# Performance work log

Hardware: AMD Instinct MI355X
Metric: run time of the kernel (lower is better)

The kernel has to match this reference:

```python
import math
import jax, jax.numpy as jnp
import numpy as np

HEADS = 8
DIM_HEAD = 64
NUM_MEM_KV = 16


def alibi_slopes(heads):
    def pow2_slopes(n):
        start = 2 ** (-(2 ** -(math.log2(n) - 3)))
        return [start * (start ** i) for i in range(n)]
    if math.log2(heads).is_integer():
        return np.asarray(pow2_slopes(heads), dtype=np.float32)
    cp2 = 2 ** math.floor(math.log2(heads))
    extra = pow2_slopes(2 * cp2)[0::2][: heads - cp2]
    return np.asarray(pow2_slopes(cp2) + extra, dtype=np.float32)


def setup_inputs() -> dict:
    key = jax.random.key(0)
    ks = jax.random.split(key, 12)
    b, n, dim = 2, 2048, 512
    h, dh, mem = HEADS, DIM_HEAD, NUM_MEM_KV
    s = 0.02  # weight init scale for numerical sanity
    return {
        "x": jax.random.normal(ks[0], (b, n, dim), jnp.float32),
        "Wq": jax.random.normal(ks[1], (dim, h * dh), jnp.float32) * s,
        "Wk": jax.random.normal(ks[2], (dim, h * dh), jnp.float32) * s,
        "Wv": jax.random.normal(ks[3], (dim, h * dh), jnp.float32) * s,
        "mem_k": jax.random.normal(ks[4], (h, mem, dh), jnp.float32),
        "mem_v": jax.random.normal(ks[5], (h, mem, dh), jnp.float32),
        "pre_proj": jax.random.normal(ks[6], (h, h), jnp.float32),
        "post_proj": jax.random.normal(ks[7], (h, h), jnp.float32),
        "head_scale_params": jnp.ones((1, h, 1, 1), jnp.float32),
        "Wout": jax.random.normal(ks[8], (h * dh, dim), jnp.float32) * s,
        "bout": jnp.zeros((dim,), jnp.float32),
    }


def reference(x, Wq, Wk, Wv, mem_k, mem_v, pre_proj, post_proj,
              head_scale_params, Wout, bout):
    b, n, dim = x.shape
    h, dh, mem = HEADS, DIM_HEAD, NUM_MEM_KV
    scale = dh ** -0.5

    def split_heads(t):  # [b,n,h*dh] -> [b,h,n,dh]
        return t.reshape(b, n, h, dh).transpose(0, 2, 1, 3)

    q = split_heads(x @ Wq)
    k = split_heads(x @ Wk)
    v = split_heads(x @ Wv)

    # prepend learned memory key/values: k,v -> [b,h,mem+n,dh]
    k = jnp.concatenate([jnp.broadcast_to(mem_k, (b, h, mem, dh)), k], axis=2)
    v = jnp.concatenate([jnp.broadcast_to(mem_v, (b, h, mem, dh)), v], axis=2)
    j = mem + n

    dots = jnp.einsum('bhid,bhjd->bhij', q, k) * scale
    # talking heads (pre-softmax)
    dots = jnp.einsum('bhij,hk->bkij', dots, pre_proj)
    # alibi relative positional bias: arange(j) * slope per head
    slopes = jnp.asarray(alibi_slopes(h))  # [h]
    dots = dots + jnp.arange(j, dtype=dots.dtype)[None, None, None, :] * slopes[None, :, None, None]
    # causal mask (mem columns always visible); mask where col-mem > row
    neg = -jnp.finfo(dots.dtype).max
    causal = (jnp.arange(j)[None, :] - mem) > jnp.arange(n)[:, None]  # [n,j]
    dots = jnp.where(causal[None, None], neg, dots)

    attn = jax.nn.softmax(dots, axis=-1)
    # talking heads (post-softmax)
    attn = jnp.einsum('bhij,hk->bkij', attn, post_proj)

    out = jnp.einsum('bhij,bhjd->bhid', attn, v)
    out = out * head_scale_params
    out = out.transpose(0, 2, 1, 3).reshape(b, n, h * dh)
    return out @ Wout + bout
```

## Files before the change

kernel.cpp:

```cpp
#include <hip/hip_runtime.h>
#include <math.h>

namespace {
constexpr int B = 2;
constexpr int N = 2048;
constexpr int DIM = 512;
constexpr int H = 8;
constexpr int MEM = 16;
constexpr int J = MEM + N;
constexpr int CHUNK = 256;
constexpr float S2 = 0.125f * 1.4426950408889634f;
constexpr size_t EPB = 17170432;
}

typedef __attribute__((ext_vector_type(8))) short short8;
typedef __attribute__((ext_vector_type(2))) float floatx2;
typedef __attribute__((ext_vector_type(4))) float floatx4;
typedef __attribute__((ext_vector_type(4))) unsigned short ushortx4;
typedef __attribute__((ext_vector_type(8))) unsigned short ushortx8;

__device__ inline unsigned short f2bf(float f) {
    unsigned int u = __float_as_uint(f);
    u += 0x7fffu + ((u >> 16) & 1u);
    return (unsigned short)(u >> 16);
}
__device__ inline unsigned int pk2bf(float a, float b) {
    return ((__float_as_uint(a) + 0x8000u) >> 16) |
           ((__float_as_uint(b) + 0x8000u) & 0xffff0000u);
}

__global__ __launch_bounds__(256)
void x_conv(const float* __restrict__ x, unsigned short* __restrict__ x16)
{
    const size_t base = ((size_t)blockIdx.x * 256 + threadIdx.x) * 8;
    const float4 a = *(const float4*)(x + base);
    const float4 b = *(const float4*)(x + base + 4);
    ushortx8 o = { f2bf(a.x), f2bf(a.y), f2bf(a.z), f2bf(a.w),
                   f2bf(b.x), f2bf(b.y), f2bf(b.z), f2bf(b.w) };
    *(ushortx8*)(x16 + base) = o;
}

__global__ __launch_bounds__(256)
void wt_conv(const float* __restrict__ Wq, const float* __restrict__ Wk,
             const float* __restrict__ Wv, const float* __restrict__ Wo,
             unsigned short* __restrict__ tq, unsigned short* __restrict__ tk,
             unsigned short* __restrict__ tv, unsigned short* __restrict__ to_)
{
    const int z = blockIdx.z;
    const float* __restrict__ W = (z == 0) ? Wq : (z == 1) ? Wk : (z == 2) ? Wv : Wo;
    unsigned short* __restrict__ WT = (z == 0) ? tq : (z == 1) ? tk : (z == 2) ? tv : to_;
    const int k0 = blockIdx.x * 64, n0 = blockIdx.y * 64;

    __shared__ __align__(16) unsigned short tile[64][72];
    const int t = threadIdx.x;
    const int rrow = t >> 4, rcol = (t & 15) * 4;
#pragma unroll
    for (int rr = 0; rr < 4; ++rr) {
        const int row = rrow + rr * 16;
        const float4 v = *(const float4*)(W + (size_t)(k0 + row) * DIM + n0 + rcol);
        tile[rcol + 0][row] = f2bf(v.x);
        tile[rcol + 1][row] = f2bf(v.y);
        tile[rcol + 2][row] = f2bf(v.z);
        tile[rcol + 3][row] = f2bf(v.w);
    }
    __syncthreads();
    const int orow = t >> 2, oseg = (t & 3) * 16;
    *(ushortx8*)(WT + (size_t)(n0 + orow) * DIM + k0 + oseg) =
        *(const ushortx8*)(&tile[orow][oseg]);
    *(ushortx8*)(WT + (size_t)(n0 + orow) * DIM + k0 + oseg + 8) =
        *(const ushortx8*)(&tile[orow][oseg + 8]);
}

__global__ __launch_bounds__(256)
void qkv_gemm(const unsigned short* __restrict__ x16, const unsigned short* __restrict__ tq,
              const unsigned short* __restrict__ tk, const unsigned short* __restrict__ tv,
              unsigned short* __restrict__ q16, unsigned short* __restrict__ k16,
              unsigned short* __restrict__ vt16)
{
    const int which = blockIdx.z;
    const unsigned short* __restrict__ WT = (which == 0) ? tq : (which == 1) ? tk : tv;
    const int t = threadIdx.x;
    const int lane = t & 63, w = t >> 6;
    const int iL = lane & 15, quad = lane >> 4;
    const int mb = blockIdx.x * 64;
    const int n0 = blockIdx.y * 64;

    __shared__ __align__(16) unsigned short As[2][64][32];
    __shared__ __align__(16) unsigned short Bs[2][64][32];

    const int r0 = t >> 2, s8 = (t & 3) * 8;

    floatx4 acc[4];
#pragma unroll
    for (int ng = 0; ng < 4; ++ng) acc[ng] = (floatx4){0.f, 0.f, 0.f, 0.f};

    {
        *(ushortx8*)(&As[0][r0][s8]) =
            *(const ushortx8*)(x16 + (size_t)(mb + r0) * DIM + s8);
        *(ushortx8*)(&Bs[0][r0][s8]) =
            *(const ushortx8*)(WT + (size_t)(n0 + r0) * DIM + s8);
    }
    __syncthreads();

#pragma unroll
    for (int it = 0; it < 16; ++it) {
        const int buf = it & 1;
        if (it + 1 < 16) {
            const int k0 = (it + 1) * 32;
            const ushortx8 av = *(const ushortx8*)(x16 + (size_t)(mb + r0) * DIM + k0 + s8);
            const ushortx8 bv = *(const ushortx8*)(WT + (size_t)(n0 + r0) * DIM + k0 + s8);
            *(ushortx8*)(&As[buf ^ 1][r0][s8]) = av;
            *(ushortx8*)(&Bs[buf ^ 1][r0][s8]) = bv;
        }
        const short8 af = *(const short8*)(&As[buf][w * 16 + iL][quad * 8]);
#pragma unroll
        for (int ng = 0; ng < 4; ++ng) {
            const short8 bf = *(const short8*)(&Bs[buf][ng * 16 + iL][quad * 8]);
            acc[ng] = __builtin_amdgcn_mfma_f32_16x16x32_bf16(af, bf, acc[ng], 0, 0, 0);
        }
        __syncthreads();
    }

    const int mbw = mb + w * 16;
    const int h0 = n0 >> 6;
    if (which == 2) {
#pragma unroll
        for (int ng = 0; ng < 4; ++ng) {
            const int d = ng * 16 + iL;
#pragma unroll
            for (int r = 0; r < 4; ++r) {
                const int m = mbw + quad * 4 + r;
                const int bb = m >> 11, ii = m & (N - 1);
                vt16[((size_t)(bb * H + h0) * 64 + d) * J + MEM + ii] = f2bf(acc[ng][r]);
            }
        }
    } else {
        unsigned short* dst = (which == 0) ? q16 : k16;
#pragma unroll
        for (int ng = 0; ng < 4; ++ng) {
            const int d = ng * 16 + iL;
#pragma unroll
            for (int r = 0; r < 4; ++r) {
                const int m = mbw + quad * 4 + r;
                const int bb = m >> 11, ii = m & (N - 1);
                const size_t rowbase = (which == 0)
                    ? ((size_t)(bb * H + h0) * N + ii)
                    : ((size_t)(bb * H + h0) * J + MEM + ii);
                dst[rowbase * 64 + d] = f2bf(acc[ng][r]);
            }
        }
    }
}

__global__ void memkv_copy(const float* __restrict__ mem_k, const float* __restrict__ mem_v,
                           unsigned short* __restrict__ k16, unsigned short* __restrict__ vt16)
{
    const int idx = blockIdx.x * 256 + threadIdx.x;
    if (idx >= H * MEM * 64) return;
    const int h0 = idx >> 10;
    const int rd = idx & 1023;
    const int r = rd >> 6, d = rd & 63;
    const unsigned short kk = f2bf(mem_k[idx]);
    const unsigned short vv = f2bf(mem_v[idx]);
#pragma unroll
    for (int bb = 0; bb < B; ++bb) {
        k16[((size_t)(bb * H + h0) * J + r) * 64 + d] = kk;
        vt16[((size_t)(bb * H + h0) * 64 + d) * J + r] = vv;
    }
}

__global__ __launch_bounds__(256)
void attn_scores(const unsigned short* __restrict__ qb, const unsigned short* __restrict__ kb,
                 const float* __restrict__ prep, float* __restrict__ lbuf,
                 unsigned short* __restrict__ e16)
{
    const int tt = blockIdx.x, c = 8 - blockIdx.y, b = blockIdx.z;
    const int i0 = tt * 16;
    const int jlim = i0 + 32;
    const int jstart = c * CHUNK;
    if (jstart >= jlim) return;
    const int jend = min(jstart + CHUNK, jlim);

    __shared__ __align__(16) unsigned short q_s[8][16][64];
    __shared__ float pre_s[64];
    const int t = threadIdx.x;
    if (t < 64) pre_s[t] = prep[t];
#pragma unroll
    for (int u4 = 0; u4 < 4; ++u4) {
        const int u = t + u4 * 256;
        const int h = u >> 7, rem = u & 127, i = rem >> 3, seg = (rem & 7) * 8;
        *(ushortx8*)(&q_s[h][i][seg ^ ((i & 7) << 3)]) =
            *(const ushortx8*)(qb + ((size_t)(b * H + h) * N + i0 + i) * 64 + seg);
    }
    __syncthreads();

    const int lane = t & 63, w = t >> 6;
    const int iL = lane & 15, quad = lane >> 4;
    const int i = i0 + iL;
    const int sw = (iL & 7) << 3;
    const size_t ebase = (size_t)b * EPB + (size_t)(8 * tt * tt + 24 * tt) * 128;

    float l_acc[8];
#pragma unroll
    for (int h1 = 0; h1 < 8; ++h1) l_acc[h1] = 0.f;

    bool any = false;
    for (int j0 = jstart + w * 16; j0 < jend; j0 += 64) {
        any = true;
        floatx2 d01[8], d23[8];
#pragma unroll
        for (int h1 = 0; h1 < 8; ++h1) {
            d01[h1] = (floatx2){0.f, 0.f};
            d23[h1] = (floatx2){0.f, 0.f};
        }

        const unsigned short* kbase = kb + ((size_t)(b * H) * J + j0 + iL) * 64 + quad * 8;
        const size_t hstride = (size_t)J * 64;
        short8 ka0 = *(const short8*)(kbase);
        short8 ka1 = *(const short8*)(kbase + 32);
        short8 kb0_ = *(const short8*)(kbase + hstride);
        short8 kb1_ = *(const short8*)(kbase + hstride + 32);
#pragma unroll
        for (int h0 = 0; h0 < 8; ++h0) {
            short8 kc0_, kc1_;
            if (h0 < 6) {
                const unsigned short* kpn = kbase + (size_t)(h0 + 2) * hstride;
                kc0_ = *(const short8*)(kpn);
                kc1_ = *(const short8*)(kpn + 32);
            }
            const short8 qf0 = *(const short8*)(&q_s[h0][iL][(quad * 8) ^ sw]);
            const short8 qf1 = *(const short8*)(&q_s[h0][iL][(quad * 8 + 32) ^ sw]);
            floatx4 a = {0.f, 0.f, 0.f, 0.f};
            a = __builtin_amdgcn_mfma_f32_16x16x32_bf16(ka0, qf0, a, 0, 0, 0);
            a = __builtin_amdgcn_mfma_f32_16x16x32_bf16(ka1, qf1, a, 0, 0, 0);
            const floatx2 av01 = {a[0], a[1]}, av23 = {a[2], a[3]};
            const float4 pr0 = *(const float4*)(&pre_s[h0 * 8]);
            const float4 pr1 = *(const float4*)(&pre_s[h0 * 8 + 4]);
            d01[0] += av01 * pr0.x;  d23[0] += av23 * pr0.x;
            d01[1] += av01 * pr0.y;  d23[1] += av23 * pr0.y;
            d01[2] += av01 * pr0.z;  d23[2] += av23 * pr0.z;
            d01[3] += av01 * pr0.w;  d23[3] += av23 * pr0.w;
            d01[4] += av01 * pr1.x;  d23[4] += av23 * pr1.x;
            d01[5] += av01 * pr1.y;  d23[5] += av23 * pr1.y;
            d01[6] += av01 * pr1.z;  d23[6] += av23 * pr1.z;
            d01[7] += av01 * pr1.w;  d23[7] += av23 * pr1.w;
            ka0 = kb0_; ka1 = kb1_; kb0_ = kc0_; kb1_ = kc1_;
        }

        unsigned int epk[4][4];
        float etmp[4];
#pragma unroll
        for (int h1 = 0; h1 < 8; ++h1) {
            const float slopeE = 1.4426950408889634f / (float)(2 << h1);
            const float dd0 = d01[h1][0], dd1 = d01[h1][1];
            const float dd2 = d23[h1][0], dd3 = d23[h1][1];
#pragma unroll
            for (int r = 0; r < 4; ++r) {
                const float dv = (r == 0) ? dd0 : (r == 1) ? dd1 : (r == 2) ? dd2 : dd3;
                const int j = j0 + quad * 4 + r;
                const bool vis = (j - MEM) <= i;
                const float e = vis ? exp2f(fmaf(dv, S2, slopeE * (float)(j - i - MEM)))
                                    : 0.f;
                l_acc[h1] += e;
                if (h1 & 1) epk[r][h1 >> 1] = pk2bf(etmp[r], e);
                else        etmp[r] = e;
            }
        }
#pragma unroll
        for (int r = 0; r < 4; ++r) {
            uint4 o = make_uint4(epk[r][0], epk[r][1], epk[r][2], epk[r][3]);
            *(uint4*)(e16 + ebase + (size_t)((j0 + quad * 4 + r) * 16 + iL) * 8) = o;
        }
    }

#pragma unroll
    for (int h1 = 0; h1 < 8; ++h1) {
        float v = l_acc[h1];
        v += __shfl_xor(v, 16);
        v += __shfl_xor(v, 32);
        if (quad == 0 && any)
            atomicAdd(lbuf + ((size_t)(b * 128 + tt) * 8 + h1) * 16 + iL, v);
    }
}

__global__ __launch_bounds__(256)
void attn_pv2(const unsigned short* __restrict__ e16, const unsigned short* __restrict__ vt,
              const float* __restrict__ postp, const float* __restrict__ hsp,
              const float* __restrict__ lbuf, float* __restrict__ ao)
{
    const int tt = blockIdx.x, c = 8 - blockIdx.y, b = blockIdx.z;
    const int i0 = tt * 16;
    const int jlim = i0 + 32;
    const int jstart = c * CHUNK;
    if (jstart >= jlim) return;
    const int jend = min(jstart + CHUNK, jlim);
    const int nw = (jend - jstart + 31) >> 5;

    __shared__ __align__(16) unsigned short p2s[2][8][16][40];
    __shared__ __align__(16) float post_s[64];

    const int t = threadIdx.x;
    if (t < 64) post_s[t] = postp[t] * hsp[t & 7];

    const int lane = t & 63, w = t >> 6;
    const int iL = lane & 15, quad = lane >> 4;
    const int dW = w * 16 + iL;
    const int i_p = t & 15;
    const int jj = t >> 4;
    const size_t ebase = (size_t)b * EPB + (size_t)(8 * tt * tt + 24 * tt) * 128;
    const unsigned short* __restrict__ ep = e16 + ebase + (size_t)i_p * 8;

    float linv[8];
#pragma unroll
    for (int h1 = 0; h1 < 8; ++h1)
        linv[h1] = 1.0f / lbuf[((size_t)(b * 128 + tt) * 8 + h1) * 16 + i_p];

    floatx4 y[8];
#pragma unroll
    for (int h2 = 0; h2 < 8; ++h2) y[h2] = (floatx4){0.f, 0.f, 0.f, 0.f};

    ushortx8 evA[2], evB[2], evC[2];
    {
        const int j0c = jstart + jj * 2;
        int ja = min(j0c, jend - 1), jb2 = min(j0c + 1, jend - 1);
        evA[0] = *(const ushortx8*)(ep + (size_t)(ja * 16) * 8);
        evA[1] = *(const ushortx8*)(ep + (size_t)(jb2 * 16) * 8);
        ja = min(j0c + 32, jend - 1); jb2 = min(j0c + 33, jend - 1);
        evB[0] = *(const ushortx8*)(ep + (size_t)(ja * 16) * 8);
        evB[1] = *(const ushortx8*)(ep + (size_t)(jb2 * 16) * 8);
        ja = min(j0c + 64, jend - 1); jb2 = min(j0c + 65, jend - 1);
        evC[0] = *(const ushortx8*)(ep + (size_t)(ja * 16) * 8);
        evC[1] = *(const ushortx8*)(ep + (size_t)(jb2 * 16) * 8);
    }
    __syncthreads();

    for (int n = 0; n < nw; ++n) {
        const int jw0 = jstart + n * 32;
        const int buf = n & 1;

        int jbv = jw0 + quad * 8;
        if (jbv > J - 8) jbv = J - 8;
        short8 bF[8];
#pragma unroll
        for (int h2 = 0; h2 < 8; ++h2)
            bF[h2] = *(const short8*)(vt + ((size_t)(b * H + h2) * 64 + dW) * J + jbv);

        ushortx8 evT0, evT1;
        {
            const int wn = (n + 3 < nw) ? n + 3 : nw - 1;
            const int j0n = jstart + wn * 32 + jj * 2;
            const int ja = min(j0n, jend - 1), jb2 = min(j0n + 1, jend - 1);
            evT0 = *(const ushortx8*)(ep + (size_t)(ja * 16) * 8);
            evT1 = *(const ushortx8*)(ep + (size_t)(jb2 * 16) * 8);
        }

        floatx2 p2v[2][4];
#pragma unroll
        for (int s = 0; s < 2; ++s) {
#pragma unroll
            for (int q = 0; q < 4; ++q) p2v[s][q] = (floatx2){0.f, 0.f};
            const int j = jw0 + jj * 2 + s;
            if (j < jend) {
#pragma unroll
                for (int h1 = 0; h1 < 8; ++h1) {
                    const float e = __uint_as_float(
                        (unsigned int)(unsigned short)evA[s][h1] << 16) * linv[h1];
                    const floatx2* po = (const floatx2*)(&post_s[h1 * 8]);
                    p2v[s][0] += e * po[0];
                    p2v[s][1] += e * po[1];
                    p2v[s][2] += e * po[2];
                    p2v[s][3] += e * po[3];
                }
            }
        }
#pragma unroll
        for (int h2 = 0; h2 < 8; ++h2)
            *(unsigned int*)(&p2s[buf][h2][i_p][jj * 2]) =
                pk2bf(p2v[0][h2 >> 1][h2 & 1], p2v[1][h2 >> 1][h2 & 1]);
        __syncthreads();

#pragma unroll
        for (int h2 = 0; h2 < 8; ++h2) {
            const short8 aF = *(const short8*)(&p2s[buf][h2][iL][quad * 8]);
            y[h2] = __builtin_amdgcn_mfma_f32_16x16x32_bf16(aF, bF[h2], y[h2], 0, 0, 0);
        }
        evA[0] = evB[0]; evA[1] = evB[1];
        evB[0] = evC[0]; evB[1] = evC[1];
        evC[0] = evT0;   evC[1] = evT1;
    }

#pragma unroll
    for (int h2 = 0; h2 < 8; ++h2) {
#pragma unroll
        for (int r = 0; r < 4; ++r) {
            const int ii = i0 + quad * 4 + r;
            atomicAdd(ao + ((size_t)b * N + ii) * DIM + h2 * 64 + dW, y[h2][r]);
        }
    }
}

__global__ __launch_bounds__(256)
void out_gemm(const float* __restrict__ ain, const unsigned short* __restrict__ WT,
              const float* __restrict__ bo, float* __restrict__ out)
{
    const int t = threadIdx.x;
    const int lane = t & 63, w = t >> 6;
    const int iL = lane & 15, quad = lane >> 4;
    const int mb = blockIdx.x * 64;
    const int n0 = blockIdx.y * 64;

    __shared__ __align__(16) unsigned short As[2][64][32];
    __shared__ __align__(16) unsigned short Bs[2][64][32];

    const int ar0 = t >> 3, as4 = (t & 7) * 4;
    const int br0 = t >> 2, bs8 = (t & 3) * 8;

    floatx4 acc[4];
#pragma unroll
    for (int ng = 0; ng < 4; ++ng) acc[ng] = (floatx4){0.f, 0.f, 0.f, 0.f};

    {
        const float4 v0 = *(const float4*)(ain + (size_t)(mb + ar0) * DIM + as4);
        const float4 v1 = *(const float4*)(ain + (size_t)(mb + ar0 + 32) * DIM + as4);
        ushortx4 o0 = { f2bf(v0.x), f2bf(v0.y), f2bf(v0.z), f2bf(v0.w) };
        ushortx4 o1 = { f2bf(v1.x), f2bf(v1.y), f2bf(v1.z), f2bf(v1.w) };
        *(ushortx4*)(&As[0][ar0][as4]) = o0;
        *(ushortx4*)(&As[0][ar0 + 32][as4]) = o1;
        *(ushortx8*)(&Bs[0][br0][bs8]) =
            *(const ushortx8*)(WT + (size_t)(n0 + br0) * DIM + bs8);
    }
    __syncthreads();

#pragma unroll
    for (int it = 0; it < 16; ++it) {
        const int buf = it & 1;
        if (it + 1 < 16) {
            const int k0 = (it + 1) * 32;
            const float4 v0 = *(const float4*)(ain + (size_t)(mb + ar0) * DIM + k0 + as4);
            const float4 v1 = *(const float4*)(ain + (size_t)(mb + ar0 + 32) * DIM + k0 + as4);
            const ushortx8 bv =
                *(const ushortx8*)(WT + (size_t)(n0 + br0) * DIM + k0 + bs8);
            ushortx4 o0 = { f2bf(v0.x), f2bf(v0.y), f2bf(v0.z), f2bf(v0.w) };
            ushortx4 o1 = { f2bf(v1.x), f2bf(v1.y), f2bf(v1.z), f2bf(v1.w) };
            *(ushortx4*)(&As[buf ^ 1][ar0][as4]) = o0;
            *(ushortx4*)(&As[buf ^ 1][ar0 + 32][as4]) = o1;
            *(ushortx8*)(&Bs[buf ^ 1][br0][bs8]) = bv;
        }
        const short8 af = *(const short8*)(&As[buf][w * 16 + iL][quad * 8]);
#pragma unroll
        for (int ng = 0; ng < 4; ++ng) {
            const short8 bf = *(const short8*)(&Bs[buf][ng * 16 + iL][quad * 8]);
            acc[ng] = __builtin_amdgcn_mfma_f32_16x16x32_bf16(af, bf, acc[ng], 0, 0, 0);
        }
        __syncthreads();
    }

    const int mbw = mb + w * 16;
#pragma unroll
    for (int ng = 0; ng < 4; ++ng) {
        const int n = n0 + ng * 16 + iL;
        const float bias = bo[n];
#pragma unroll
        for (int r = 0; r < 4; ++r) {
            const int m = mbw + quad * 4 + r;
            out[(size_t)m * DIM + n] = acc[ng][r] + bias;
        }
    }
}

extern "C" void kernel_launch(void* const* d_in, const int* in_sizes, int n_in,
                              void* d_out, int out_size, void* d_ws, size_t ws_size,
                              hipStream_t stream)
{
    (void)in_sizes; (void)n_in; (void)out_size; (void)ws_size;
    const float* x      = (const float*)d_in[0];
    const float* Wq     = (const float*)d_in[1];
    const float* Wk     = (const float*)d_in[2];
    const float* Wv     = (const float*)d_in[3];
    const float* mem_k  = (const float*)d_in[4];
    const float* mem_v  = (const float*)d_in[5];
    const float* pre_p  = (const float*)d_in[6];
    const float* post_p = (const float*)d_in[7];
    const float* hs     = (const float*)d_in[8];
    const float* Wo     = (const float*)d_in[9];
    const float* bo     = (const float*)d_in[10];
    float* out = (float*)d_out;

    constexpr size_t NAO  = (size_t)B * N * DIM;
    constexpr size_t NLB  = (size_t)B * 128 * H * 16;
    constexpr size_t NW   = (size_t)DIM * DIM;
    constexpr size_t NQ   = (size_t)B * H * N * 64;
    constexpr size_t NK   = (size_t)B * H * J * 64;
    constexpr size_t NX   = (size_t)B * N * DIM;

    float* ws = (float*)d_ws;
    float* ao   = ws;
    float* lbuf = ao + NAO;
    unsigned short* wtq  = (unsigned short*)(lbuf + NLB);
    unsigned short* wtk  = wtq + NW;
    unsigned short* wtv  = wtk + NW;
    unsigned short* wto  = wtv + NW;
    unsigned short* q16  = wto + NW;
    unsigned short* k16  = q16 + NQ;
    unsigned short* v16  = k16 + NK;
    unsigned short* x16  = v16 + NK;
    unsigned short* e16  = x16 + NX;

    x_conv<<<dim3(1024), 256, 0, stream>>>(x, x16);
    wt_conv<<<dim3(8, 8, 4), 256, 0, stream>>>(Wq, Wk, Wv, Wo, wtq, wtk, wtv, wto);
    qkv_gemm<<<dim3(64, 8, 3), 256, 0, stream>>>(x16, wtq, wtk, wtv, q16, k16, v16);
    memkv_copy<<<dim3(32), 256, 0, stream>>>(mem_k, mem_v, k16, v16);
    hipMemsetAsync(ao, 0, (NAO + NLB) * sizeof(float), stream);
    attn_scores<<<dim3(128, 9, B), 256, 0, stream>>>(q16, k16, pre_p, lbuf, e16);
    attn_pv2<<<dim3(128, 9, B), 256, 0, stream>>>(e16, v16, post_p, hs, lbuf, ao);
    out_gemm<<<dim3(64, 8), 256, 0, stream>>>(ao, wto, bo, out);
}
```

Baseline: 244.3 us.

## Fold pre-softmax talking-heads into Q and stage head-concatenated K via LDS

K is now stored as [b, j, h*dh] with all heads concatenated per key. The pre-softmax head mixing is folded into per-wave scaled Q fragments, so each wave computes two output heads directly with K=512 MFMA reductions. K tiles are double-buffered into LDS with global_load_lds, using an XOR swizzle, and shared across all four waves. This removes the per-head FP mixing and redundant per-wave K loads, but rounds the pre-proj-scaled Q to bf16, which changes precision, and adds a block sync per 16-key window.

```diff
diff --git a/kernel.cpp b/kernel.cpp
--- a/kernel.cpp
+++ b/kernel.cpp
@@ -18,6 +18,7 @@
 typedef __attribute__((ext_vector_type(4))) float floatx4;
 typedef __attribute__((ext_vector_type(4))) unsigned short ushortx4;
 typedef __attribute__((ext_vector_type(8))) unsigned short ushortx8;
+typedef __attribute__((ext_vector_type(4))) unsigned int uintx4;
 
 __device__ inline unsigned short f2bf(float f) {
     unsigned int u = __float_as_uint(f);
@@ -74,7 +75,7 @@
 __global__ __launch_bounds__(256)
 void qkv_gemm(const unsigned short* __restrict__ x16, const unsigned short* __restrict__ tq,
               const unsigned short* __restrict__ tk, const unsigned short* __restrict__ tv,
-              unsigned short* __restrict__ q16, unsigned short* __restrict__ k16,
+              unsigned short* __restrict__ q16, unsigned short* __restrict__ kcat,
               unsigned short* __restrict__ vt16)
 {
     const int which = blockIdx.z;
@@ -134,8 +135,7 @@
                 vt16[((size_t)(bb * H + h0) * 64 + d) * J + MEM + ii] = f2bf(acc[ng][r]);
             }
         }
-    } else {
-        unsigned short* dst = (which == 0) ? q16 : k16;
+    } else if (which == 1) {
 #pragma unroll
         for (int ng = 0; ng < 4; ++ng) {
             const int d = ng * 16 + iL;
@@ -143,17 +143,25 @@
             for (int r = 0; r < 4; ++r) {
                 const int m = mbw + quad * 4 + r;
                 const int bb = m >> 11, ii = m & (N - 1);
-                const size_t rowbase = (which == 0)
-                    ? ((size_t)(bb * H + h0) * N + ii)
-                    : ((size_t)(bb * H + h0) * J + MEM + ii);
-                dst[rowbase * 64 + d] = f2bf(acc[ng][r]);
+                kcat[((size_t)bb * J + MEM + ii) * 512 + h0 * 64 + d] = f2bf(acc[ng][r]);
             }
         }
+    } else {
+#pragma unroll
+        for (int ng = 0; ng < 4; ++ng) {
+            const int d = ng * 16 + iL;
+#pragma unroll
+            for (int r = 0; r < 4; ++r) {
+                const int m = mbw + quad * 4 + r;
+                const int bb = m >> 11, ii = m & (N - 1);
+                q16[((size_t)(bb * H + h0) * N + ii) * 64 + d] = f2bf(acc[ng][r]);
+            }
+        }
     }
 }
 
 __global__ void memkv_copy(const float* __restrict__ mem_k, const float* __restrict__ mem_v,
-                           unsigned short* __restrict__ k16, unsigned short* __restrict__ vt16)
+                           unsigned short* __restrict__ kcat, unsigned short* __restrict__ vt16)
 {
     const int idx = blockIdx.x * 256 + threadIdx.x;
     if (idx >= H * MEM * 64) return;
@@ -164,13 +172,13 @@
     const unsigned short vv = f2bf(mem_v[idx]);
 #pragma unroll
     for (int bb = 0; bb < B; ++bb) {
-        k16[((size_t)(bb * H + h0) * J + r) * 64 + d] = kk;
+        kcat[((size_t)bb * J + r) * 512 + h0 * 64 + d] = kk;
         vt16[((size_t)(bb * H + h0) * 64 + d) * J + r] = vv;
     }
 }
 
 __global__ __launch_bounds__(256)
-void attn_scores(const unsigned short* __restrict__ qb, const unsigned short* __restrict__ kb,
+void attn_scores(const unsigned short* __restrict__ qb, const unsigned short* __restrict__ kc,
                  const float* __restrict__ prep, float* __restrict__ lbuf,
                  unsigned short* __restrict__ e16)
 {
@@ -180,106 +188,103 @@
     const int jstart = c * CHUNK;
     if (jstart >= jlim) return;
     const int jend = min(jstart + CHUNK, jlim);
-
-    __shared__ __align__(16) unsigned short q_s[8][16][64];
+    const int nwin = (jend - jstart) >> 4;
+
+    __shared__ __align__(16) unsigned short k_s[2][16][512];
+    __shared__ __align__(16) unsigned short q_s[16][520];
     __shared__ float pre_s[64];
+
     const int t = threadIdx.x;
-    if (t < 64) pre_s[t] = prep[t];
-#pragma unroll
-    for (int u4 = 0; u4 < 4; ++u4) {
-        const int u = t + u4 * 256;
-        const int h = u >> 7, rem = u & 127, i = rem >> 3, seg = (rem & 7) * 8;
-        *(ushortx8*)(&q_s[h][i][seg ^ ((i & 7) << 3)]) =
-            *(const ushortx8*)(qb + ((size_t)(b * H + h) * N + i0 + i) * 64 + seg);
-    }
-    __syncthreads();
-
     const int lane = t & 63, w = t >> 6;
     const int iL = lane & 15, quad = lane >> 4;
     const int i = i0 + iL;
-    const int sw = (iL & 7) << 3;
+
+    const size_t krowbase = (size_t)b * J * 512;
+
+    auto STAGE = [&](int buf, int jw0) {
+#pragma unroll
+        for (int rr = 0; rr < 4; ++rr) {
+            const int row = rr * 4 + w;
+            const int j = jw0 + row;
+            const char* src = (const char*)(kc + krowbase + (size_t)j * 512);
+            const int soff = (lane * 16) ^ ((j & 7) << 4);
+            __builtin_amdgcn_global_load_lds(
+                (const __attribute__((address_space(1))) unsigned int*)(src + soff),
+                (__attribute__((address_space(3))) unsigned int*)(&k_s[buf][row][0]),
+                16, 0, 0);
+        }
+    };
+
+    if (t < 64) pre_s[t] = prep[t];
+#pragma unroll
+    for (int k4 = 0; k4 < 4; ++k4) {
+        const int ch = t + k4 * 256;
+        const int qi = ch >> 6, cc = ch & 63;
+        const int h0 = cc >> 3, seg = (cc & 7) * 8;
+        *(ushortx8*)(&q_s[qi][cc * 8]) =
+            *(const ushortx8*)(qb + ((size_t)(b * H + h0) * N + i0 + qi) * 64 + seg);
+    }
+    STAGE(0, jstart);
+    __syncthreads();
+
+    const int h1a = 2 * w, h1b = 2 * w + 1;
+    short8 qfA[16], qfB[16];
+#pragma unroll
+    for (int ks = 0; ks < 16; ++ks) {
+        const int h0 = ks >> 1;
+        const float sA = pre_s[h0 * 8 + h1a];
+        const float sB = pre_s[h0 * 8 + h1b];
+        const ushortx8 raw = *(const ushortx8*)(&q_s[iL][ks * 32 + quad * 8]);
+        uintx4 ua, ub;
+#pragma unroll
+        for (int e2 = 0; e2 < 4; ++e2) {
+            const float f0 = __uint_as_float((unsigned int)raw[e2 * 2] << 16);
+            const float f1 = __uint_as_float((unsigned int)raw[e2 * 2 + 1] << 16);
+            ua[e2] = pk2bf(f0 * sA, f1 * sA);
+            ub[e2] = pk2bf(f0 * sB, f1 * sB);
+        }
+        qfA[ks] = __builtin_bit_cast(short8, ua);
+        qfB[ks] = __builtin_bit_cast(short8, ub);
+    }
+
+    const float slA = 1.4426950408889634f / (float)(2 << h1a);
+    const float slB = 1.4426950408889634f / (float)(2 << h1b);
     const size_t ebase = (size_t)b * EPB + (size_t)(8 * tt * tt + 24 * tt) * 128;
-
-    float l_acc[8];
-#pragma unroll
-    for (int h1 = 0; h1 < 8; ++h1) l_acc[h1] = 0.f;
-
-    bool any = false;
-    for (int j0 = jstart + w * 16; j0 < jend; j0 += 64) {
-        any = true;
-        floatx2 d01[8], d23[8];
-#pragma unroll
-        for (int h1 = 0; h1 < 8; ++h1) {
-            d01[h1] = (floatx2){0.f, 0.f};
-            d23[h1] = (floatx2){0.f, 0.f};
-        }
-
-        const unsigned short* kbase = kb + ((size_t)(b * H) * J + j0 + iL) * 64 + quad * 8;
-        const size_t hstride = (size_t)J * 64;
-        short8 ka0 = *(const short8*)(kbase);
-        short8 ka1 = *(const short8*)(kbase + 32);
-        short8 kb0_ = *(const short8*)(kbase + hstride);
-        short8 kb1_ = *(const short8*)(kbase + hstride + 32);
-#pragma unroll
-        for (int h0 = 0; h0 < 8; ++h0) {
-            short8 kc0_, kc1_;
-            if (h0 < 6) {
-                const unsigned short* kpn = kbase + (size_t)(h0 + 2) * hstride;
-                kc0_ = *(const short8*)(kpn);
-                kc1_ = *(const short8*)(kpn + 32);
-            }
-            const short8 qf0 = *(const short8*)(&q_s[h0][iL][(quad * 8) ^ sw]);
-            const short8 qf1 = *(const short8*)(&q_s[h0][iL][(quad * 8 + 32) ^ sw]);
-            floatx4 a = {0.f, 0.f, 0.f, 0.f};
-            a = __builtin_amdgcn_mfma_f32_16x16x32_bf16(ka0, qf0, a, 0, 0, 0);
-            a = __builtin_amdgcn_mfma_f32_16x16x32_bf16(ka1, qf1, a, 0, 0, 0);
-            const floatx2 av01 = {a[0], a[1]}, av23 = {a[2], a[3]};
-            const float4 pr0 = *(const float4*)(&pre_s[h0 * 8]);
-            const float4 pr1 = *(const float4*)(&pre_s[h0 * 8 + 4]);
-            d01[0] += av01 * pr0.x;  d23[0] += av23 * pr0.x;
-            d01[1] += av01 * pr0.y;  d23[1] += av23 * pr0.y;
-            d01[2] += av01 * pr0.z;  d23[2] += av23 * pr0.z;
-            d01[3] += av01 * pr0.w;  d23[3] += av23 * pr0.w;
-            d01[4] += av01 * pr1.x;  d23[4] += av23 * pr1.x;
-            d01[5] += av01 * pr1.y;  d23[5] += av23 * pr1.y;
-            d01[6] += av01 * pr1.z;  d23[6] += av23 * pr1.z;
-            d01[7] += av01 * pr1.w;  d23[7] += av23 * pr1.w;
-            ka0 = kb0_; ka1 = kb1_; kb0_ = kc0_; kb1_ = kc1_;
-        }
-
-        unsigned int epk[4][4];
-        float etmp[4];
-#pragma unroll
-        for (int h1 = 0; h1 < 8; ++h1) {
-            const float slopeE = 1.4426950408889634f / (float)(2 << h1);
-            const float dd0 = d01[h1][0], dd1 = d01[h1][1];
-            const float dd2 = d23[h1][0], dd3 = d23[h1][1];
-#pragma unroll
-            for (int r = 0; r < 4; ++r) {
-                const float dv = (r == 0) ? dd0 : (r == 1) ? dd1 : (r == 2) ? dd2 : dd3;
-                const int j = j0 + quad * 4 + r;
-                const bool vis = (j - MEM) <= i;
-                const float e = vis ? exp2f(fmaf(dv, S2, slopeE * (float)(j - i - MEM)))
-                                    : 0.f;
-                l_acc[h1] += e;
-                if (h1 & 1) epk[r][h1 >> 1] = pk2bf(etmp[r], e);
-                else        etmp[r] = e;
-            }
-        }
+    float l0 = 0.f, l1 = 0.f;
+
+    for (int n = 0; n < nwin; ++n) {
+        const int buf = n & 1;
+        if (n + 1 < nwin) STAGE(buf ^ 1, jstart + (n + 1) * 16);
+        const int jw0 = jstart + n * 16;
+
+        floatx4 a0 = {0.f, 0.f, 0.f, 0.f}, a1 = {0.f, 0.f, 0.f, 0.f};
+#pragma unroll
+        for (int ks = 0; ks < 16; ++ks) {
+            const int off = (ks * 32 + quad * 8) ^ ((iL & 7) << 3);
+            const short8 aF = *(const short8*)(&k_s[buf][iL][off]);
+            a0 = __builtin_amdgcn_mfma_f32_16x16x32_bf16(aF, qfA[ks], a0, 0, 0, 0);
+            a1 = __builtin_amdgcn_mfma_f32_16x16x32_bf16(aF, qfB[ks], a1, 0, 0, 0);
+        }
+
 #pragma unroll
         for (int r = 0; r < 4; ++r) {
-            uint4 o = make_uint4(epk[r][0], epk[r][1], epk[r][2], epk[r][3]);
-            *(uint4*)(e16 + ebase + (size_t)((j0 + quad * 4 + r) * 16 + iL) * 8) = o;
-        }
-    }
-
-#pragma unroll
-    for (int h1 = 0; h1 < 8; ++h1) {
-        float v = l_acc[h1];
-        v += __shfl_xor(v, 16);
-        v += __shfl_xor(v, 32);
-        if (quad == 0 && any)
-            atomicAdd(lbuf + ((size_t)(b * 128 + tt) * 8 + h1) * 16 + iL, v);
+            const int j = jw0 + quad * 4 + r;
+            const int jm = j - MEM;
+            const bool vis = jm <= i;
+            const float bias = (float)(jm - i);
+            const float e0 = vis ? exp2f(fmaf(a0[r], S2, slA * bias)) : 0.f;
+            const float e1 = vis ? exp2f(fmaf(a1[r], S2, slB * bias)) : 0.f;
+            l0 += e0; l1 += e1;
+            *(unsigned int*)(e16 + ebase + ((size_t)j * 16 + iL) * 8 + h1a) = pk2bf(e0, e1);
+        }
+        __syncthreads();
+    }
+
+    l0 += __shfl_xor(l0, 16); l0 += __shfl_xor(l0, 32);
+    l1 += __shfl_xor(l1, 16); l1 += __shfl_xor(l1, 32);
+    if (quad == 0) {
+        atomicAdd(lbuf + ((size_t)(b * 128 + tt) * 8 + h1a) * 16 + iL, l0);
+        atomicAdd(lbuf + ((size_t)(b * 128 + tt) * 8 + h1b) * 16 + iL, l1);
     }
 }
 
@@ -490,7 +495,7 @@
     constexpr size_t NLB  = (size_t)B * 128 * H * 16;
     constexpr size_t NW   = (size_t)DIM * DIM;
     constexpr size_t NQ   = (size_t)B * H * N * 64;
-    constexpr size_t NK   = (size_t)B * H * J * 64;
+    constexpr size_t NK   = (size_t)B * J * 512;
     constexpr size_t NX   = (size_t)B * N * DIM;
 
     float* ws = (float*)d_ws;
@@ -501,17 +506,17 @@
     unsigned short* wtv  = wtk + NW;
     unsigned short* wto  = wtv + NW;
     unsigned short* q16  = wto + NW;
-    unsigned short* k16  = q16 + NQ;
-    unsigned short* v16  = k16 + NK;
+    unsigned short* kcat = q16 + NQ;
+    unsigned short* v16  = kcat + NK;
     unsigned short* x16  = v16 + NK;
     unsigned short* e16  = x16 + NX;
 
     x_conv<<<dim3(1024), 256, 0, stream>>>(x, x16);
     wt_conv<<<dim3(8, 8, 4), 256, 0, stream>>>(Wq, Wk, Wv, Wo, wtq, wtk, wtv, wto);
-    qkv_gemm<<<dim3(64, 8, 3), 256, 0, stream>>>(x16, wtq, wtk, wtv, q16, k16, v16);
-    memkv_copy<<<dim3(32), 256, 0, stream>>>(mem_k, mem_v, k16, v16);
+    qkv_gemm<<<dim3(64, 8, 3), 256, 0, stream>>>(x16, wtq, wtk, wtv, q16, kcat, v16);
+    memkv_copy<<<dim3(32), 256, 0, stream>>>(mem_k, mem_v, kcat, v16);
     hipMemsetAsync(ao, 0, (NAO + NLB) * sizeof(float), stream);
-    attn_scores<<<dim3(128, 9, B), 256, 0, stream>>>(q16, k16, pre_p, lbuf, e16);
+    attn_scores<<<dim3(128, 9, B), 256, 0, stream>>>(q16, kcat, pre_p, lbuf, e16);
     attn_pv2<<<dim3(128, 9, B), 256, 0, stream>>>(e16, v16, post_p, hs, lbuf, ao);
     out_gemm<<<dim3(64, 8), 256, 0, stream>>>(ao, wto, bo, out);
 }
```

After: 234.8 us. 1.04x faster.

## Reorder attention grid to heavy-rows-first and simplify score kernel register pipeline

Applied to the files above, without the earlier changes.

Swaps the grid mapping of the scores and PV kernels so chunks are the fast index and row tiles run in reverse order, scheduling the longest causal rows first. Blocks for one row tile also sit next to each other in launch order. The scores kernel drops the LDS XOR swizzle on Q, switching to a plain row layout that may cause bank conflicts. It also cuts K prefetch depth from two heads to one and replaces the paired floatx2 accumulators with scalar FMAs. Together these aim to reduce tail imbalance and register pressure, at the cost of possible LDS conflicts and less latency hiding.

```diff
diff --git a/kernel.cpp b/kernel.cpp
--- a/kernel.cpp
+++ b/kernel.cpp
@@ -9,6 +9,7 @@
 constexpr int MEM = 16;
 constexpr int J = MEM + N;
 constexpr int CHUNK = 256;
+constexpr int CMAX = 9;
 constexpr float S2 = 0.125f * 1.4426950408889634f;
 constexpr size_t EPB = 17170432;
 }
@@ -174,7 +175,7 @@
                  const float* __restrict__ prep, float* __restrict__ lbuf,
                  unsigned short* __restrict__ e16)
 {
-    const int tt = blockIdx.x, c = 8 - blockIdx.y, b = blockIdx.z;
+    const int c = blockIdx.x, tt = 127 - blockIdx.y, b = blockIdx.z;
     const int i0 = tt * 16;
     const int jlim = i0 + 32;
     const int jstart = c * CHUNK;
@@ -182,14 +183,14 @@
     const int jend = min(jstart + CHUNK, jlim);
 
     __shared__ __align__(16) unsigned short q_s[8][16][64];
-    __shared__ float pre_s[64];
+    __shared__ __align__(16) float pre_s[64];
     const int t = threadIdx.x;
     if (t < 64) pre_s[t] = prep[t];
 #pragma unroll
     for (int u4 = 0; u4 < 4; ++u4) {
         const int u = t + u4 * 256;
         const int h = u >> 7, rem = u & 127, i = rem >> 3, seg = (rem & 7) * 8;
-        *(ushortx8*)(&q_s[h][i][seg ^ ((i & 7) << 3)]) =
+        *(ushortx8*)(&q_s[h][i][seg]) =
             *(const ushortx8*)(qb + ((size_t)(b * H + h) * N + i0 + i) * 64 + seg);
     }
     __syncthreads();
@@ -197,7 +198,6 @@
     const int lane = t & 63, w = t >> 6;
     const int iL = lane & 15, quad = lane >> 4;
     const int i = i0 + iL;
-    const int sw = (iL & 7) << 3;
     const size_t ebase = (size_t)b * EPB + (size_t)(8 * tt * tt + 24 * tt) * 128;
 
     float l_acc[8];
@@ -207,44 +207,44 @@
     bool any = false;
     for (int j0 = jstart + w * 16; j0 < jend; j0 += 64) {
         any = true;
-        floatx2 d01[8], d23[8];
-#pragma unroll
-        for (int h1 = 0; h1 < 8; ++h1) {
-            d01[h1] = (floatx2){0.f, 0.f};
-            d23[h1] = (floatx2){0.f, 0.f};
-        }
-
-        const unsigned short* kbase = kb + ((size_t)(b * H) * J + j0 + iL) * 64 + quad * 8;
-        const size_t hstride = (size_t)J * 64;
-        short8 ka0 = *(const short8*)(kbase);
-        short8 ka1 = *(const short8*)(kbase + 32);
-        short8 kb0_ = *(const short8*)(kbase + hstride);
-        short8 kb1_ = *(const short8*)(kbase + hstride + 32);
+        float dots[8][4];
+#pragma unroll
+        for (int h1 = 0; h1 < 8; ++h1)
+#pragma unroll
+            for (int r = 0; r < 4; ++r) dots[h1][r] = 0.f;
+
+        const unsigned short* kp0 = kb + ((size_t)(b * H) * J + j0 + iL) * 64 + quad * 8;
+        short8 kc0 = *(const short8*)kp0;
+        short8 kc1 = *(const short8*)(kp0 + 32);
 #pragma unroll
         for (int h0 = 0; h0 < 8; ++h0) {
-            short8 kc0_, kc1_;
-            if (h0 < 6) {
-                const unsigned short* kpn = kbase + (size_t)(h0 + 2) * hstride;
-                kc0_ = *(const short8*)(kpn);
-                kc1_ = *(const short8*)(kpn + 32);
+            short8 kn0, kn1;
+            if (h0 < 7) {
+                const unsigned short* kpn =
+                    kb + ((size_t)(b * H + h0 + 1) * J + j0 + iL) * 64 + quad * 8;
+                kn0 = *(const short8*)kpn;
+                kn1 = *(const short8*)(kpn + 32);
             }
-            const short8 qf0 = *(const short8*)(&q_s[h0][iL][(quad * 8) ^ sw]);
-            const short8 qf1 = *(const short8*)(&q_s[h0][iL][(quad * 8 + 32) ^ sw]);
+            const short8 qf0 = *(const short8*)(&q_s[h0][iL][quad * 8]);
+            const short8 qf1 = *(const short8*)(&q_s[h0][iL][quad * 8 + 32]);
             floatx4 a = {0.f, 0.f, 0.f, 0.f};
-            a = __builtin_amdgcn_mfma_f32_16x16x32_bf16(ka0, qf0, a, 0, 0, 0);
-            a = __builtin_amdgcn_mfma_f32_16x16x32_bf16(ka1, qf1, a, 0, 0, 0);
-            const floatx2 av01 = {a[0], a[1]}, av23 = {a[2], a[3]};
+            a = __builtin_amdgcn_mfma_f32_16x16x32_bf16(kc0, qf0, a, 0, 0, 0);
+            a = __builtin_amdgcn_mfma_f32_16x16x32_bf16(kc1, qf1, a, 0, 0, 0);
             const float4 pr0 = *(const float4*)(&pre_s[h0 * 8]);
             const float4 pr1 = *(const float4*)(&pre_s[h0 * 8 + 4]);
-            d01[0] += av01 * pr0.x;  d23[0] += av23 * pr0.x;
-            d01[1] += av01 * pr0.y;  d23[1] += av23 * pr0.y;
-            d01[2] += av01 * pr0.z;  d23[2] += av23 * pr0.z;
-            d01[3] += av01 * pr0.w;  d23[3] += av23 * pr0.w;
-            d01[4] += av01 * pr1.x;  d23[4] += av23 * pr1.x;
-            d01[5] += av01 * pr1.y;  d23[5] += av23 * pr1.y;
-            d01[6] += av01 * pr1.z;  d23[6] += av23 * pr1.z;
-            d01[7] += av01 * pr1.w;  d23[7] += av23 * pr1.w;
-            ka0 = kb0_; ka1 = kb1_; kb0_ = kc0_; kb1_ = kc1_;
+#pragma unroll
+            for (int r = 0; r < 4; ++r) {
+                const float av = a[r];
+                dots[0][r] = fmaf(av, pr0.x, dots[0][r]);
+                dots[1][r] = fmaf(av, pr0.y, dots[1][r]);
+                dots[2][r] = fmaf(av, pr0.z, dots[2][r]);
+                dots[3][r] = fmaf(av, pr0.w, dots[3][r]);
+                dots[4][r] = fmaf(av, pr1.x, dots[4][r]);
+                dots[5][r] = fmaf(av, pr1.y, dots[5][r]);
+                dots[6][r] = fmaf(av, pr1.z, dots[6][r]);
+                dots[7][r] = fmaf(av, pr1.w, dots[7][r]);
+            }
+            kc0 = kn0; kc1 = kn1;
         }
 
         unsigned int epk[4][4];
@@ -252,14 +252,11 @@
 #pragma unroll
         for (int h1 = 0; h1 < 8; ++h1) {
             const float slopeE = 1.4426950408889634f / (float)(2 << h1);
-            const float dd0 = d01[h1][0], dd1 = d01[h1][1];
-            const float dd2 = d23[h1][0], dd3 = d23[h1][1];
 #pragma unroll
             for (int r = 0; r < 4; ++r) {
-                const float dv = (r == 0) ? dd0 : (r == 1) ? dd1 : (r == 2) ? dd2 : dd3;
                 const int j = j0 + quad * 4 + r;
                 const bool vis = (j - MEM) <= i;
-                const float e = vis ? exp2f(fmaf(dv, S2, slopeE * (float)(j - i - MEM)))
+                const float e = vis ? exp2f(fmaf(dots[h1][r], S2, slopeE * (float)(j - i - MEM)))
                                     : 0.f;
                 l_acc[h1] += e;
                 if (h1 & 1) epk[r][h1 >> 1] = pk2bf(etmp[r], e);
@@ -288,7 +285,7 @@
               const float* __restrict__ postp, const float* __restrict__ hsp,
               const float* __restrict__ lbuf, float* __restrict__ ao)
 {
-    const int tt = blockIdx.x, c = 8 - blockIdx.y, b = blockIdx.z;
+    const int c = blockIdx.x, tt = 127 - blockIdx.y, b = blockIdx.z;
     const int i0 = tt * 16;
     const int jlim = i0 + 32;
     const int jstart = c * CHUNK;
@@ -511,7 +508,7 @@
     qkv_gemm<<<dim3(64, 8, 3), 256, 0, stream>>>(x16, wtq, wtk, wtv, q16, k16, v16);
     memkv_copy<<<dim3(32), 256, 0, stream>>>(mem_k, mem_v, k16, v16);
     hipMemsetAsync(ao, 0, (NAO + NLB) * sizeof(float), stream);
-    attn_scores<<<dim3(128, 9, B), 256, 0, stream>>>(q16, k16, pre_p, lbuf, e16);
-    attn_pv2<<<dim3(128, 9, B), 256, 0, stream>>>(e16, v16, post_p, hs, lbuf, ao);
+    attn_scores<<<dim3(CMAX, 128, B), 256, 0, stream>>>(q16, k16, pre_p, lbuf, e16);
+    attn_pv2<<<dim3(CMAX, 128, B), 256, 0, stream>>>(e16, v16, post_p, hs, lbuf, ao);
     out_gemm<<<dim3(64, 8), 256, 0, stream>>>(ao, wto, bo, out);
 }
```

Result: faster. 226.0 us (-7.5%).
